# Optimization experiments

Hardware: AMD Instinct MI355X
Metric: run time of the kernel (lower is better)

Reference implementation:

```python
import jax, jax.numpy as jnp
import numpy as np

B, ISIZE, HSIZE = 256, 256, 512
CLIPVAL = 2.0

def _linear(x, W, b):
    # torch nn.Linear: y = x @ W.T + b, W is [out, in]
    return x @ W.T + b

def setup_inputs() -> dict:
    key = jax.random.key(0)
    ks = jax.random.split(key, 24)
    d = {}
    d['inputs'] = jax.random.normal(ks[0], (B, ISIZE), jnp.float32)
    d['h0'] = jax.random.normal(ks[1], (B, HSIZE), jnp.float32) * 0.1
    d['c0'] = jax.random.normal(ks[2], (B, HSIZE), jnp.float32) * 0.1
    d['hebb'] = jax.random.normal(ks[3], (B, HSIZE, HSIZE), jnp.float32) * 0.01
    d['w'] = 0.02 * jax.random.uniform(ks[4], (HSIZE, HSIZE), jnp.float32) - 0.01
    d['alpha'] = 0.0001 * jax.random.uniform(ks[5], (1, 1, HSIZE), jnp.float32)
    scale_h = 1.0 / np.sqrt(HSIZE)
    scale_i = 1.0 / np.sqrt(ISIZE)
    d['h2f_w'] = jax.random.uniform(ks[6], (HSIZE, HSIZE), jnp.float32, -scale_h, scale_h)
    d['h2f_b'] = jax.random.uniform(ks[7], (HSIZE,), jnp.float32, -scale_h, scale_h)
    d['h2i_w'] = jax.random.uniform(ks[8], (HSIZE, HSIZE), jnp.float32, -scale_h, scale_h)
    d['h2i_b'] = jax.random.uniform(ks[9], (HSIZE,), jnp.float32, -scale_h, scale_h)
    d['h2opt_w'] = jax.random.uniform(ks[10], (HSIZE, HSIZE), jnp.float32, -scale_h, scale_h)
    d['h2opt_b'] = jax.random.uniform(ks[11], (HSIZE,), jnp.float32, -scale_h, scale_h)
    d['x2f_w'] = jax.random.uniform(ks[12], (HSIZE, ISIZE), jnp.float32, -scale_i, scale_i)
    d['x2f_b'] = jax.random.uniform(ks[13], (HSIZE,), jnp.float32, -scale_i, scale_i)
    d['x2i_w'] = jax.random.uniform(ks[14], (HSIZE, ISIZE), jnp.float32, -scale_i, scale_i)
    d['x2i_b'] = jax.random.uniform(ks[15], (HSIZE,), jnp.float32, -scale_i, scale_i)
    d['x2opt_w'] = jax.random.uniform(ks[16], (HSIZE, ISIZE), jnp.float32, -scale_i, scale_i)
    d['x2opt_b'] = jax.random.uniform(ks[17], (HSIZE,), jnp.float32, -scale_i, scale_i)
    d['x2c_w'] = jax.random.uniform(ks[18], (HSIZE, ISIZE), jnp.float32, -scale_i, scale_i)
    d['x2c_b'] = jax.random.uniform(ks[19], (HSIZE,), jnp.float32, -scale_i, scale_i)
    d['h2mod_w'] = jax.random.uniform(ks[20], (1, HSIZE), jnp.float32, -scale_h, scale_h)
    d['h2mod_b'] = jax.random.uniform(ks[21], (1,), jnp.float32, -scale_h, scale_h)
    d['modfanout_w'] = jax.random.uniform(ks[22], (HSIZE, 1), jnp.float32, -1.0, 1.0)
    d['modfanout_b'] = jax.random.uniform(ks[23], (HSIZE,), jnp.float32, -1.0, 1.0)
    return d

def reference(inputs, h0, c0, hebb, w, alpha,
              h2f_w, h2f_b, h2i_w, h2i_b, h2opt_w, h2opt_b,
              x2f_w, x2f_b, x2i_w, x2i_b, x2opt_w, x2opt_b, x2c_w, x2c_b,
              h2mod_w, h2mod_b, modfanout_w, modfanout_b):
    # gates
    fgt = jax.nn.sigmoid(_linear(inputs, x2f_w, x2f_b) + _linear(h0, h2f_w, h2f_b))
    ipt = jax.nn.sigmoid(_linear(inputs, x2i_w, x2i_b) + _linear(h0, h2i_w, h2i_b))
    opt = jax.nn.sigmoid(_linear(inputs, x2opt_w, x2opt_b) + _linear(h0, h2opt_w, h2opt_b))
    # plastic recurrent matmul: h [B,h] x (w + alpha*hebb) [B,h,h]
    M = w[None, :, :] + alpha * hebb  # [B, h, h]
    h2coutput = jnp.einsum('bh,bhk->bk', h0, M)
    inputstocell = jnp.tanh(_linear(inputs, x2c_w, x2c_b) + h2coutput)
    cell = fgt * c0 + ipt * inputstocell
    hactiv = opt * jnp.tanh(cell)
    # Hebbian outer product (hebboutput='i2c')
    deltahebb = h0[:, :, None] * inputstocell[:, None, :]  # [B, h, h]
    # modulation: modultype='modplasth2mod', modulout='fanout'
    m = jnp.tanh(_linear(hactiv, h2mod_w, h2mod_b))  # [B, 1]
    fan = m[:, 0][:, None] * modfanout_w[:, 0][None, :] + modfanout_b[None, :]  # [B, h]
    myeta = fan[:, None, :]  # [B, 1, h]
    # cliptype='clip'
    hebb_new = jnp.clip(hebb + myeta * deltahebb, -CLIPVAL, CLIPVAL)
    return hactiv, cell, hebb_new
```

## Files before the change

### kernel.cpp

```cpp
#include <hip/hip_runtime.h>
#include <math.h>

#define BATCH 256
#define ISZ 256
#define H 512
#define BH (BATCH * H)
#define CLIPV 2.0f

typedef float f4_t __attribute__((ext_vector_type(4)));

__device__ __forceinline__ float sigmoidf_(float x) { return 1.0f / (1.0f + expf(-x)); }
__device__ __forceinline__ f4_t nt_load4(const f4_t* p) { return __builtin_nontemporal_load(p); }
__device__ __forceinline__ void nt_store4(f4_t* p, f4_t v) { __builtin_nontemporal_store(v, p); }

#define BT 64
#define KT 32
#define LDSP (BT + 4)
#define NGEMM 160
#define NEIN  2048

__global__ __launch_bounds__(256) void gemms_einsum(
    const float* __restrict__ x, const float* __restrict__ h0,
    const float* __restrict__ x2f_w, const float* __restrict__ x2f_b,
    const float* __restrict__ h2f_w, const float* __restrict__ h2f_b,
    const float* __restrict__ x2i_w, const float* __restrict__ x2i_b,
    const float* __restrict__ h2i_w, const float* __restrict__ h2i_b,
    const float* __restrict__ x2o_w, const float* __restrict__ x2o_b,
    const float* __restrict__ h2o_w, const float* __restrict__ h2o_b,
    const float* __restrict__ x2c_w, const float* __restrict__ x2c_b,
    const float* __restrict__ w,
    const float* __restrict__ hebb,
    float* __restrict__ pre, float* __restrict__ hbpart)
{
  __shared__ __align__(16) float As[KT][LDSP];
  __shared__ __align__(16) float Bs[KT][LDSP];
  __shared__ float h0s[64];
  __shared__ f4_t redv[128];

  const int bid = blockIdx.x;
  const int t   = threadIdx.x;

  if (bid >= NGEMM) {
    const int e    = bid - NGEMM;
    const int b    = e >> 3;
    const int hseg = e & 7;
    const int col  = t & 127;
    const int half = t >> 7;
    if (t < 64) h0s[t] = h0[b * H + hseg * 64 + t];
    __syncthreads();
    const f4_t* hb4 = (const f4_t*)hebb +
        (size_t)(b * H + hseg * 64 + half * 32) * (H / 4);
    f4_t acc = {0.f, 0.f, 0.f, 0.f};
    #pragma unroll 8
    for (int h = 0; h < 32; ++h) {
      f4_t v = hb4[(size_t)h * 128 + col];
      float s = h0s[half * 32 + h];
      acc += s * v;
    }
    if (half == 1) redv[col] = acc;
    __syncthreads();
    if (half == 0) {
      acc += redv[col];
      ((f4_t*)hbpart)[(size_t)(b * 8 + hseg) * 128 + col] = acc;
    }
    return;
  }

  const int z   = bid >> 5;
  const int rem = bid & 31;
  const int n0  = (rem & 7) * BT;
  const int m0  = (rem >> 3) * BT;
  const int tx = t & 15, ty = t >> 4;

  float acc[4][4] = {{0.0f}};

  const float* Aseg[2]; const float* Bseg[2];
  int ldaS[2], KS[2]; int nseg; bool kmajor = true;
  const float* xb = nullptr; const float* hbias = nullptr;

  if (z < 3) {
    const float* xw; const float* hw_;
    if (z == 0)      { xw = x2f_w; xb = x2f_b; hw_ = h2f_w; hbias = h2f_b; }
    else if (z == 1) { xw = x2i_w; xb = x2i_b; hw_ = h2i_w; hbias = h2i_b; }
    else             { xw = x2o_w; xb = x2o_b; hw_ = h2o_w; hbias = h2o_b; }
    Aseg[0] = x;  ldaS[0] = ISZ; Bseg[0] = xw;  KS[0] = ISZ;
    Aseg[1] = h0; ldaS[1] = H;   Bseg[1] = hw_; KS[1] = H;
    nseg = 2;
  } else if (z == 3) {
    Aseg[0] = x; ldaS[0] = ISZ; Bseg[0] = x2c_w; KS[0] = ISZ; xb = x2c_b;
    nseg = 1;
  } else {
    Aseg[0] = h0; ldaS[0] = H; Bseg[0] = w; KS[0] = H;
    nseg = 1; kmajor = false;
  }

  for (int s = 0; s < nseg; ++s) {
    const float* A  = Aseg[s];
    const float* Bm = Bseg[s];
    const int lda = ldaS[s];
    const int K   = KS[s];
    for (int kk0 = 0; kk0 < K; kk0 += KT) {
      #pragma unroll
      for (int i = 0; i < 8; ++i) {
        int l = i * 256 + t;
        int j = l & 31, r = l >> 5;
        As[j][r] = A[(size_t)(m0 + r) * lda + kk0 + j];
      }
      if (kmajor) {
        #pragma unroll
        for (int i = 0; i < 8; ++i) {
          int l = i * 256 + t;
          int j = l & 31, n = l >> 5;
          Bs[j][n] = Bm[(size_t)(n0 + n) * K + kk0 + j];
        }
      } else {
        #pragma unroll
        for (int i = 0; i < 8; ++i) {
          int l = i * 256 + t;
          int n = l & 63, j = l >> 6;
          Bs[j][n] = Bm[(size_t)(kk0 + j) * H + n0 + n];
        }
      }
      __syncthreads();
      #pragma unroll
      for (int j = 0; j < KT; ++j) {
        float4 a  = *(const float4*)&As[j][ty * 4];
        float4 bv = *(const float4*)&Bs[j][tx * 4];
        float av[4] = {a.x, a.y, a.z, a.w};
        float bw[4] = {bv.x, bv.y, bv.z, bv.w};
        #pragma unroll
        for (int r = 0; r < 4; ++r)
          #pragma unroll
          for (int c = 0; c < 4; ++c)
            acc[r][c] += av[r] * bw[c];
      }
      __syncthreads();
    }
  }

  float bias[4];
  #pragma unroll
  for (int c = 0; c < 4; ++c) {
    int n = n0 + tx * 4 + c;
    float bv = 0.0f;
    if (z < 3)       bv = xb[n] + hbias[n];
    else if (z == 3) bv = xb[n];
    bias[c] = bv;
  }
  float* outc = pre + (size_t)z * BH;
  #pragma unroll
  for (int r = 0; r < 4; ++r) {
    int m = m0 + ty * 4 + r;
    float4 o;
    o.x = acc[r][0] + bias[0];
    o.y = acc[r][1] + bias[1];
    o.z = acc[r][2] + bias[2];
    o.w = acc[r][3] + bias[3];
    *(float4*)&outc[(size_t)m * H + n0 + tx * 4] = o;
  }
}

__global__ __launch_bounds__(256) void fuse_mod(
    const float* __restrict__ pre, const float* __restrict__ hbpart,
    const float* __restrict__ c0, const float* __restrict__ alpha,
    const float* __restrict__ h2mod_w, const float* __restrict__ h2mod_b,
    const float* __restrict__ mfo_w, const float* __restrict__ mfo_b,
    float* __restrict__ out, float* __restrict__ eta)
{
  const int b = blockIdx.x, t = threadIdx.x;
  float ha[2], itcv[2];
  #pragma unroll
  for (int u = 0; u < 2; ++u) {
    const int k   = t + u * 256;
    const int idx = b * H + k;
    float hb = 0.0f;
    #pragma unroll
    for (int s = 0; s < 8; ++s) hb += hbpart[(size_t)(b * 8 + s) * H + k];
    float h2c = pre[(size_t)4 * BH + idx] + alpha[k] * hb;
    float it  = tanhf(pre[(size_t)3 * BH + idx] + h2c);
    float f = sigmoidf_(pre[idx]);
    float i = sigmoidf_(pre[(size_t)BH + idx]);
    float o = sigmoidf_(pre[(size_t)2 * BH + idx]);
    float cell = f * c0[idx] + i * it;
    float h = o * tanhf(cell);
    out[idx] = h;
    out[BH + idx] = cell;
    ha[u] = h; itcv[u] = it;
  }
  float s = ha[0] * h2mod_w[t] + ha[1] * h2mod_w[t + 256];
  #pragma unroll
  for (int off = 32; off > 0; off >>= 1) s += __shfl_down(s, off, 64);
  __shared__ float red[4];
  __shared__ float mm;
  if ((t & 63) == 0) red[t >> 6] = s;
  __syncthreads();
  if (t == 0) mm = tanhf(red[0] + red[1] + red[2] + red[3] + h2mod_b[0]);
  __syncthreads();
  float m = mm;
  #pragma unroll
  for (int u = 0; u < 2; ++u) {
    const int k = t + u * 256;
    eta[b * H + k] = (m * mfo_w[k] + mfo_b[k]) * itcv[u];
  }
}

__global__ __launch_bounds__(256) void hebb_update(
    const float* __restrict__ hebb, const float* __restrict__ h0,
    const float* __restrict__ eta, float* __restrict__ out)
{
  const size_t g = (size_t)(gridDim.x - 1 - blockIdx.x) * 256 + threadIdx.x;
  f4_t v = nt_load4((const f4_t*)hebb + g);
  const int k4  = (int)(g & 127);
  const int row = (int)(g >> 7);
  const int b   = row >> 9;
  f4_t e = ((const f4_t*)eta)[(b << 7) + k4];
  float s = h0[row];
  f4_t r;
  r.x = fminf(fmaxf(v.x + s * e.x, -CLIPV), CLIPV);
  r.y = fminf(fmaxf(v.y + s * e.y, -CLIPV), CLIPV);
  r.z = fminf(fmaxf(v.z + s * e.z, -CLIPV), CLIPV);
  r.w = fminf(fmaxf(v.w + s * e.w, -CLIPV), CLIPV);
  nt_store4((f4_t*)out + (size_t)(2 * BH / 4) + g, r);
}

extern "C" void kernel_launch(void* const* d_in, const int* in_sizes, int n_in,
                              void* d_out, int out_size, void* d_ws, size_t ws_size,
                              hipStream_t stream) {
  const float* x       = (const float*)d_in[0];
  const float* h0      = (const float*)d_in[1];
  const float* c0      = (const float*)d_in[2];
  const float* hebb    = (const float*)d_in[3];
  const float* w       = (const float*)d_in[4];
  const float* alpha   = (const float*)d_in[5];
  const float* h2f_w   = (const float*)d_in[6];
  const float* h2f_b   = (const float*)d_in[7];
  const float* h2i_w   = (const float*)d_in[8];
  const float* h2i_b   = (const float*)d_in[9];
  const float* h2o_w   = (const float*)d_in[10];
  const float* h2o_b   = (const float*)d_in[11];
  const float* x2f_w   = (const float*)d_in[12];
  const float* x2f_b   = (const float*)d_in[13];
  const float* x2i_w   = (const float*)d_in[14];
  const float* x2i_b   = (const float*)d_in[15];
  const float* x2o_w   = (const float*)d_in[16];
  const float* x2o_b   = (const float*)d_in[17];
  const float* x2c_w   = (const float*)d_in[18];
  const float* x2c_b   = (const float*)d_in[19];
  const float* h2mod_w = (const float*)d_in[20];
  const float* h2mod_b = (const float*)d_in[21];
  const float* mfo_w   = (const float*)d_in[22];
  const float* mfo_b   = (const float*)d_in[23];

  float* out = (float*)d_out;
  float* ws  = (float*)d_ws;

  float* pre    = ws;
  float* hbpart = pre + (size_t)5 * BH;
  float* eta    = hbpart + (size_t)BATCH * 8 * H;

  gemms_einsum<<<NGEMM + NEIN, 256, 0, stream>>>(
      x, h0, x2f_w, x2f_b, h2f_w, h2f_b, x2i_w, x2i_b, h2i_w, h2i_b,
      x2o_w, x2o_b, h2o_w, h2o_b, x2c_w, x2c_b, w, hebb, pre, hbpart);

  fuse_mod<<<BATCH, 256, 0, stream>>>(
      pre, hbpart, c0, alpha, h2mod_w, h2mod_b, mfo_w, mfo_b, out, eta);

  hebb_update<<<(BH * (H / 4)) / 256, 256, 0, stream>>>(hebb, h0, eta, out);
}
```

Before: 628.9 us.

## Split gate GEMMs per input, vectorize tile loads, coarsen einsum blocks

The three gate GEMMs, which each ran the x and h0 K-segments in sequence inside one block, are split into separate blocks per weight matrix. That gives 8 independent GEMM outputs whose partial sums are added in the fuse kernel. Global-to-LDS tile loads change from scalar to float4 loads. Each einsum block now covers 128 hebb rows instead of 64, which halves the partial buffer and the block count. The aim is to balance GEMM work across more blocks and cut load instruction count, at the cost of extra workspace traffic for the split pre-activations.

```diff
diff --git a/kernel.cpp b/kernel.cpp
--- a/kernel.cpp
+++ b/kernel.cpp
@@ -16,8 +16,8 @@
 #define BT 64
 #define KT 32
 #define LDSP (BT + 4)
-#define NGEMM 160
-#define NEIN  2048
+#define NGEMM 256
+#define NEIN  1024
 
 __global__ __launch_bounds__(256) void gemms_einsum(
     const float* __restrict__ x, const float* __restrict__ h0,
@@ -34,7 +34,7 @@
 {
   __shared__ __align__(16) float As[KT][LDSP];
   __shared__ __align__(16) float Bs[KT][LDSP];
-  __shared__ float h0s[64];
+  __shared__ float h0s[128];
   __shared__ f4_t redv[128];
 
   const int bid = blockIdx.x;
@@ -42,100 +42,90 @@
 
   if (bid >= NGEMM) {
     const int e    = bid - NGEMM;
-    const int b    = e >> 3;
-    const int hseg = e & 7;
+    const int b    = e >> 2;
+    const int seg  = e & 3;
     const int col  = t & 127;
     const int half = t >> 7;
-    if (t < 64) h0s[t] = h0[b * H + hseg * 64 + t];
+    if (t < 128) h0s[t] = h0[b * H + seg * 128 + t];
     __syncthreads();
     const f4_t* hb4 = (const f4_t*)hebb +
-        (size_t)(b * H + hseg * 64 + half * 32) * (H / 4);
+        (size_t)(b * H + seg * 128 + half * 64) * (H / 4) + col;
     f4_t acc = {0.f, 0.f, 0.f, 0.f};
     #pragma unroll 8
-    for (int h = 0; h < 32; ++h) {
-      f4_t v = hb4[(size_t)h * 128 + col];
-      float s = h0s[half * 32 + h];
-      acc += s * v;
+    for (int h = 0; h < 64; ++h) {
+      acc += h0s[half * 64 + h] * hb4[(size_t)h * 128];
     }
     if (half == 1) redv[col] = acc;
     __syncthreads();
     if (half == 0) {
       acc += redv[col];
-      ((f4_t*)hbpart)[(size_t)(b * 8 + hseg) * 128 + col] = acc;
+      ((f4_t*)hbpart)[(size_t)(b * 4 + seg) * 128 + col] = acc;
     }
     return;
   }
 
-  const int z   = bid >> 5;
+  const int ch  = bid >> 5;
   const int rem = bid & 31;
   const int n0  = (rem & 7) * BT;
   const int m0  = (rem >> 3) * BT;
   const int tx = t & 15, ty = t >> 4;
 
+  const float* A; const float* Bm; int lda, K; bool kmajor = true;
+  const float* b1 = nullptr; const float* b2 = nullptr;
+  switch (ch) {
+    case 0: A = x;  lda = ISZ; K = ISZ; Bm = x2f_w; b1 = x2f_b; b2 = h2f_b; break;
+    case 1: A = h0; lda = H;   K = H;   Bm = h2f_w; break;
+    case 2: A = x;  lda = ISZ; K = ISZ; Bm = x2i_w; b1 = x2i_b; b2 = h2i_b; break;
+    case 3: A = h0; lda = H;   K = H;   Bm = h2i_w; break;
+    case 4: A = x;  lda = ISZ; K = ISZ; Bm = x2o_w; b1 = x2o_b; b2 = h2o_b; break;
+    case 5: A = h0; lda = H;   K = H;   Bm = h2o_w; break;
+    case 6: A = x;  lda = ISZ; K = ISZ; Bm = x2c_w; b1 = x2c_b; break;
+    default: A = h0; lda = H;  K = H;   Bm = w; kmajor = false; break;
+  }
+
   float acc[4][4] = {{0.0f}};
 
-  const float* Aseg[2]; const float* Bseg[2];
-  int ldaS[2], KS[2]; int nseg; bool kmajor = true;
-  const float* xb = nullptr; const float* hbias = nullptr;
-
-  if (z < 3) {
-    const float* xw; const float* hw_;
-    if (z == 0)      { xw = x2f_w; xb = x2f_b; hw_ = h2f_w; hbias = h2f_b; }
-    else if (z == 1) { xw = x2i_w; xb = x2i_b; hw_ = h2i_w; hbias = h2i_b; }
-    else             { xw = x2o_w; xb = x2o_b; hw_ = h2o_w; hbias = h2o_b; }
-    Aseg[0] = x;  ldaS[0] = ISZ; Bseg[0] = xw;  KS[0] = ISZ;
-    Aseg[1] = h0; ldaS[1] = H;   Bseg[1] = hw_; KS[1] = H;
-    nseg = 2;
-  } else if (z == 3) {
-    Aseg[0] = x; ldaS[0] = ISZ; Bseg[0] = x2c_w; KS[0] = ISZ; xb = x2c_b;
-    nseg = 1;
-  } else {
-    Aseg[0] = h0; ldaS[0] = H; Bseg[0] = w; KS[0] = H;
-    nseg = 1; kmajor = false;
-  }
-
-  for (int s = 0; s < nseg; ++s) {
-    const float* A  = Aseg[s];
-    const float* Bm = Bseg[s];
-    const int lda = ldaS[s];
-    const int K   = KS[s];
-    for (int kk0 = 0; kk0 < K; kk0 += KT) {
+  for (int kk0 = 0; kk0 < K; kk0 += KT) {
+    #pragma unroll
+    for (int i = 0; i < 2; ++i) {
+      int l = i * 256 + t;
+      int r = l >> 3, c = l & 7;
+      float4 v = *(const float4*)&A[(size_t)(m0 + r) * lda + kk0 + c * 4];
+      As[c * 4 + 0][r] = v.x; As[c * 4 + 1][r] = v.y;
+      As[c * 4 + 2][r] = v.z; As[c * 4 + 3][r] = v.w;
+    }
+    if (kmajor) {
       #pragma unroll
-      for (int i = 0; i < 8; ++i) {
+      for (int i = 0; i < 2; ++i) {
         int l = i * 256 + t;
-        int j = l & 31, r = l >> 5;
-        As[j][r] = A[(size_t)(m0 + r) * lda + kk0 + j];
+        int n = l >> 3, c = l & 7;
+        float4 v = *(const float4*)&Bm[(size_t)(n0 + n) * K + kk0 + c * 4];
+        Bs[c * 4 + 0][n] = v.x; Bs[c * 4 + 1][n] = v.y;
+        Bs[c * 4 + 2][n] = v.z; Bs[c * 4 + 3][n] = v.w;
       }
-      if (kmajor) {
+    } else {
+      #pragma unroll
+      for (int i = 0; i < 2; ++i) {
+        int l = i * 256 + t;
+        int j = l >> 4, c = l & 15;
+        float4 v = *(const float4*)&Bm[(size_t)(kk0 + j) * H + n0 + c * 4];
+        *(float4*)&Bs[j][c * 4] = v;
+      }
+    }
+    __syncthreads();
+    #pragma unroll
+    for (int j = 0; j < KT; ++j) {
+      float4 a  = *(const float4*)&As[j][ty * 4];
+      float4 bv = *(const float4*)&Bs[j][tx * 4];
+      float av[4] = {a.x, a.y, a.z, a.w};
+      float bw[4] = {bv.x, bv.y, bv.z, bv.w};
+      #pragma unroll
+      for (int r = 0; r < 4; ++r)
         #pragma unroll
-        for (int i = 0; i < 8; ++i) {
-          int l = i * 256 + t;
-          int j = l & 31, n = l >> 5;
-          Bs[j][n] = Bm[(size_t)(n0 + n) * K + kk0 + j];
-        }
-      } else {
-        #pragma unroll
-        for (int i = 0; i < 8; ++i) {
-          int l = i * 256 + t;
-          int n = l & 63, j = l >> 6;
-          Bs[j][n] = Bm[(size_t)(kk0 + j) * H + n0 + n];
-        }
-      }
-      __syncthreads();
-      #pragma unroll
-      for (int j = 0; j < KT; ++j) {
-        float4 a  = *(const float4*)&As[j][ty * 4];
-        float4 bv = *(const float4*)&Bs[j][tx * 4];
-        float av[4] = {a.x, a.y, a.z, a.w};
-        float bw[4] = {bv.x, bv.y, bv.z, bv.w};
-        #pragma unroll
-        for (int r = 0; r < 4; ++r)
-          #pragma unroll
-          for (int c = 0; c < 4; ++c)
-            acc[r][c] += av[r] * bw[c];
-      }
-      __syncthreads();
-    }
+        for (int c = 0; c < 4; ++c)
+          acc[r][c] += av[r] * bw[c];
+    }
+    __syncthreads();
   }
 
   float bias[4];
@@ -143,11 +133,11 @@
   for (int c = 0; c < 4; ++c) {
     int n = n0 + tx * 4 + c;
     float bv = 0.0f;
-    if (z < 3)       bv = xb[n] + hbias[n];
-    else if (z == 3) bv = xb[n];
+    if (b1) bv += b1[n];
+    if (b2) bv += b2[n];
     bias[c] = bv;
   }
-  float* outc = pre + (size_t)z * BH;
+  float* outc = pre + (size_t)ch * BH;
   #pragma unroll
   for (int r = 0; r < 4; ++r) {
     int m = m0 + ty * 4 + r;
@@ -175,12 +165,12 @@
     const int idx = b * H + k;
     float hb = 0.0f;
     #pragma unroll
-    for (int s = 0; s < 8; ++s) hb += hbpart[(size_t)(b * 8 + s) * H + k];
-    float h2c = pre[(size_t)4 * BH + idx] + alpha[k] * hb;
-    float it  = tanhf(pre[(size_t)3 * BH + idx] + h2c);
-    float f = sigmoidf_(pre[idx]);
-    float i = sigmoidf_(pre[(size_t)BH + idx]);
-    float o = sigmoidf_(pre[(size_t)2 * BH + idx]);
+    for (int s = 0; s < 4; ++s) hb += hbpart[(size_t)(b * 4 + s) * H + k];
+    float h2c = pre[(size_t)7 * BH + idx] + alpha[k] * hb;
+    float it  = tanhf(pre[(size_t)6 * BH + idx] + h2c);
+    float f = sigmoidf_(pre[idx]                + pre[(size_t)1 * BH + idx]);
+    float i = sigmoidf_(pre[(size_t)2 * BH + idx] + pre[(size_t)3 * BH + idx]);
+    float o = sigmoidf_(pre[(size_t)4 * BH + idx] + pre[(size_t)5 * BH + idx]);
     float cell = f * c0[idx] + i * it;
     float h = o * tanhf(cell);
     out[idx] = h;
@@ -255,8 +245,8 @@
   float* ws  = (float*)d_ws;
 
   float* pre    = ws;
-  float* hbpart = pre + (size_t)5 * BH;
-  float* eta    = hbpart + (size_t)BATCH * 8 * H;
+  float* hbpart = pre + (size_t)8 * BH;
+  float* eta    = hbpart + (size_t)BATCH * 4 * H;
 
   gemms_einsum<<<NGEMM + NEIN, 256, 0, stream>>>(
       x, h0, x2f_w, x2f_b, h2f_w, h2f_b, x2i_w, x2i_b, h2i_w, h2i_b,
```

Result: faster. 541.1 us (-14.0%).
